# Kernel optimization log

Hardware: AMD Instinct MI355X
Metric: run time of the kernel (lower is better)

Reference implementation:

```python
import jax, jax.numpy as jnp
import numpy as np

NUM_CLASSES = 10
N = 4194304  # 2**22 samples


def setup_inputs() -> dict:
    key = jax.random.key(0)
    k1, k2 = jax.random.split(key)
    outputs = jax.random.uniform(k1, (N, NUM_CLASSES), dtype=jnp.float32)
    target = jax.random.randint(k2, (N,), 0, NUM_CLASSES, dtype=jnp.int64)
    return {"outputs": outputs, "target": target}


def reference(outputs, target):
    # y = one-hot(target) with 10 classes, float
    y = jax.nn.one_hot(target, NUM_CLASSES, dtype=outputs.dtype)  # [N, 10]
    # sum_j (outputs @ y.T)[i, j] == outputs[i] . sum_j y[j]
    # identical math to torch.sum(torch.mm(outputs, y.t()), dim=1) without the [N, N] intermediate
    col_counts = jnp.sum(y, axis=0)                 # [10] class counts
    nominator = outputs @ col_counts                # [N]
    denominator = jnp.linalg.norm(outputs) * jnp.linalg.norm(y)  # Frobenius norms
    return jnp.mean(-jnp.log(nominator / denominator))
```

## Files before the change

### kernel.cpp

```cpp
#include <hip/hip_runtime.h>
#include <math.h>

#define NUM_CLASSES 10
#define A_BLOCKS 512
#define B_BLOCKS 2048


__global__ void __launch_bounds__(256) hist_kernel(const int* __restrict__ target,
                                                   unsigned int* __restrict__ pc, int n) {
    unsigned int cnt[NUM_CLASSES];
#pragma unroll
    for (int c = 0; c < NUM_CLASSES; ++c) cnt[c] = 0u;

    const int tid = blockIdx.x * blockDim.x + threadIdx.x;
    const int stride = gridDim.x * blockDim.x;
    const int4* __restrict__ t4 = (const int4*)target;
    const int n4 = n >> 2;

    unsigned long long acc = 0ull;
    int pend = 0;
    for (int i = tid; i < n4; i += stride) {
        int4 v = t4[i];
        acc += (1ull << (6 * v.x)) + (1ull << (6 * v.y)) +
               (1ull << (6 * v.z)) + (1ull << (6 * v.w));
        if (++pend == 8) {
#pragma unroll
            for (int c = 0; c < NUM_CLASSES; ++c)
                cnt[c] += (unsigned int)((acc >> (6 * c)) & 63ull);
            acc = 0ull;
            pend = 0;
        }
    }
#pragma unroll
    for (int c = 0; c < NUM_CLASSES; ++c)
        cnt[c] += (unsigned int)((acc >> (6 * c)) & 63ull);

#pragma unroll
    for (int c = 0; c < NUM_CLASSES; ++c) {
        unsigned int v = cnt[c];
        for (int off = 32; off > 0; off >>= 1)
            v += (unsigned int)__shfl_down((int)v, off, 64);
        cnt[c] = v;
    }

    __shared__ unsigned int sh[4][NUM_CLASSES];
    const int wave = threadIdx.x >> 6;
    if ((threadIdx.x & 63) == 0) {
#pragma unroll
        for (int c = 0; c < NUM_CLASSES; ++c) sh[wave][c] = cnt[c];
    }
    __syncthreads();
    if (threadIdx.x < NUM_CLASSES) {
        const int c = threadIdx.x;
        pc[blockIdx.x * NUM_CLASSES + c] = sh[0][c] + sh[1][c] + sh[2][c] + sh[3][c];
    }
}

__device__ __forceinline__ void compute_pair(const float4 r[5], const float w[NUM_CLASSES],
                                             float& sum_log, float& sumsq) {
    float r0[NUM_CLASSES] = {r[0].x, r[0].y, r[0].z, r[0].w,
                             r[1].x, r[1].y, r[1].z, r[1].w, r[2].x, r[2].y};
    float r1[NUM_CLASSES] = {r[2].z, r[2].w, r[3].x, r[3].y,
                             r[3].z, r[3].w, r[4].x, r[4].y, r[4].z, r[4].w};
    float nom0 = 0.f, nom1 = 0.f;
#pragma unroll
    for (int c = 0; c < NUM_CLASSES; ++c) {
        nom0 += r0[c] * w[c];
        nom1 += r1[c] * w[c];
        sumsq += r0[c] * r0[c] + r1[c] * r1[c];
    }
    sum_log += __logf(nom0) + __logf(nom1);
}

__device__ __forceinline__ void process_pair_direct(const float4* __restrict__ o4, size_t p,
                                                    const float w[NUM_CLASSES],
                                                    float& sum_log, float& sumsq) {
    const float4* base = o4 + p * 5;
    float4 r[5] = {base[0], base[1], base[2], base[3], base[4]};
    compute_pair(r, w, sum_log, sumsq);
}

__global__ void __launch_bounds__(256) main_kernel(const float* __restrict__ outputs,
                                                   const unsigned int* __restrict__ pc,
                                                   float2* __restrict__ pacc, int n) {
    const int wave = threadIdx.x >> 6;
    const int lane = threadIdx.x & 63;

    unsigned int pw[NUM_CLASSES];
#pragma unroll
    for (int c = 0; c < NUM_CLASSES; ++c) pw[c] = 0u;
#pragma unroll
    for (int r = 0; r < A_BLOCKS / 256; ++r) {
        const unsigned int* row = pc + (threadIdx.x + r * 256) * NUM_CLASSES;
#pragma unroll
        for (int c = 0; c < NUM_CLASSES; ++c) pw[c] += row[c];
    }
#pragma unroll
    for (int c = 0; c < NUM_CLASSES; ++c) {
        unsigned int v = pw[c];
        for (int off = 32; off > 0; off >>= 1)
            v += (unsigned int)__shfl_down((int)v, off, 64);
        pw[c] = v;
    }
    __shared__ unsigned int shw[4][NUM_CLASSES];
    __shared__ float fw[NUM_CLASSES];
    if (lane == 0) {
#pragma unroll
        for (int c = 0; c < NUM_CLASSES; ++c) shw[wave][c] = pw[c];
    }
    __syncthreads();
    if (threadIdx.x < NUM_CLASSES) {
        const int c = threadIdx.x;
        fw[c] = (float)(shw[0][c] + shw[1][c] + shw[2][c] + shw[3][c]);
    }
    __syncthreads();
    float w[NUM_CLASSES];
#pragma unroll
    for (int c = 0; c < NUM_CLASSES; ++c) w[c] = fw[c];

    __shared__ float4 stage[4][5 * 64];
    float4* my = stage[wave];

    int wslot[5], rslot[5];
#pragma unroll
    for (int k = 0; k < 5; ++k) {
        const int j = k * 64 + lane;
        const int c = j % 5;
        const int p = j / 5;
        wslot[k] = c * 64 + (p ^ c);
        rslot[k] = k * 64 + (lane ^ k);
    }

    const float4* __restrict__ o4 = (const float4*)outputs;
    const int npairs = n >> 1;
    const int ntiles = npairs >> 6;
    const int gw = blockIdx.x * 4 + wave;
    const int nwaves = gridDim.x * 4;

    float sum_log = 0.f, sumsq = 0.f;
    for (int tile = gw; tile < ntiles; tile += nwaves) {
        const float4* src = o4 + (size_t)tile * 320;
        float4 g[5];
#pragma unroll
        for (int k = 0; k < 5; ++k) g[k] = src[k * 64 + lane];
#pragma unroll
        for (int k = 0; k < 5; ++k) my[wslot[k]] = g[k];
        float4 r[5];
#pragma unroll
        for (int k = 0; k < 5; ++k) r[k] = my[rslot[k]];
        compute_pair(r, w, sum_log, sumsq);
    }

    const int done = ntiles << 6;
    const int tid = blockIdx.x * blockDim.x + threadIdx.x;
    for (int p = done + tid; p < npairs; p += gridDim.x * blockDim.x)
        process_pair_direct(o4, (size_t)p, w, sum_log, sumsq);

    for (int off = 32; off > 0; off >>= 1) {
        sum_log += __shfl_down(sum_log, off, 64);
        sumsq += __shfl_down(sumsq, off, 64);
    }
    __shared__ float s1[4], s2[4];
    if (lane == 0) { s1[wave] = sum_log; s2[wave] = sumsq; }
    __syncthreads();
    if (threadIdx.x == 0) {
        pacc[blockIdx.x] = make_float2(s1[0] + s1[1] + s1[2] + s1[3],
                                       s2[0] + s2[1] + s2[2] + s2[3]);
    }
}

__global__ void __launch_bounds__(256) finalize_kernel(const float2* __restrict__ pacc,
                                                       float* __restrict__ out, float fn) {
    float sum_log = 0.f, sumsq = 0.f;
    for (int i = threadIdx.x; i < B_BLOCKS; i += 256) {
        float2 v = pacc[i];
        sum_log += v.x;
        sumsq += v.y;
    }
    for (int off = 32; off > 0; off >>= 1) {
        sum_log += __shfl_down(sum_log, off, 64);
        sumsq += __shfl_down(sumsq, off, 64);
    }
    __shared__ float s1[4], s2[4];
    const int wave = threadIdx.x >> 6;
    if ((threadIdx.x & 63) == 0) { s1[wave] = sum_log; s2[wave] = sumsq; }
    __syncthreads();
    if (threadIdx.x == 0) {
        float t1 = s1[0] + s1[1] + s1[2] + s1[3];
        float t2 = s2[0] + s2[1] + s2[2] + s2[3];
        out[0] = 0.5f * logf(t2) + 0.5f * logf(fn) - t1 / fn;
    }
}

extern "C" void kernel_launch(void* const* d_in, const int* in_sizes, int n_in,
                              void* d_out, int out_size, void* d_ws, size_t ws_size,
                              hipStream_t stream) {
    const float* outputs = (const float*)d_in[0];
    const int* target = (const int*)d_in[1];
    const int n = in_sizes[1];

    unsigned int* pc = (unsigned int*)d_ws;
    float2* pacc = (float2*)((char*)d_ws + 20480);

    hist_kernel<<<A_BLOCKS, 256, 0, stream>>>(target, pc, n);
    main_kernel<<<B_BLOCKS, 256, 0, stream>>>(outputs, pc, pacc, n);
    finalize_kernel<<<1, 256, 0, stream>>>(pacc, (float*)d_out, (float)n);
}
```

Before: 248.7 us.

## Fuse histogram, main pass and finalize into one cooperative kernel

Merges the three kernel launches into a single cooperative-groups kernel with 1024 blocks that uses grid-wide syncs between the class-count histogram, the per-row log/sumsq pass, and the final reduction. This removes two kernel launch gaps and their inter-kernel dependencies. It also drops the LDS-staged, swizzled tile loads in favour of direct per-thread strided float4 loads, processing two pairs per iteration. The direct loads give worse coalescing (40-byte stride per thread), and grid syncs plus the limit on co-resident blocks cost something in exchange.

```diff
diff --git a/kernel.cpp b/kernel.cpp
--- a/kernel.cpp
+++ b/kernel.cpp
@@ -1,60 +1,13 @@
 #include <hip/hip_runtime.h>
+#include <hip/hip_cooperative_groups.h>
 #include <math.h>
 
+namespace cg = cooperative_groups;
+
 #define NUM_CLASSES 10
-#define A_BLOCKS 512
-#define B_BLOCKS 2048
+#define BLOCKS 1024
+#define TPB 256
 
-
-__global__ void __launch_bounds__(256) hist_kernel(const int* __restrict__ target,
-                                                   unsigned int* __restrict__ pc, int n) {
-    unsigned int cnt[NUM_CLASSES];
-#pragma unroll
-    for (int c = 0; c < NUM_CLASSES; ++c) cnt[c] = 0u;
-
-    const int tid = blockIdx.x * blockDim.x + threadIdx.x;
-    const int stride = gridDim.x * blockDim.x;
-    const int4* __restrict__ t4 = (const int4*)target;
-    const int n4 = n >> 2;
-
-    unsigned long long acc = 0ull;
-    int pend = 0;
-    for (int i = tid; i < n4; i += stride) {
-        int4 v = t4[i];
-        acc += (1ull << (6 * v.x)) + (1ull << (6 * v.y)) +
-               (1ull << (6 * v.z)) + (1ull << (6 * v.w));
-        if (++pend == 8) {
-#pragma unroll
-            for (int c = 0; c < NUM_CLASSES; ++c)
-                cnt[c] += (unsigned int)((acc >> (6 * c)) & 63ull);
-            acc = 0ull;
-            pend = 0;
-        }
-    }
-#pragma unroll
-    for (int c = 0; c < NUM_CLASSES; ++c)
-        cnt[c] += (unsigned int)((acc >> (6 * c)) & 63ull);
-
-#pragma unroll
-    for (int c = 0; c < NUM_CLASSES; ++c) {
-        unsigned int v = cnt[c];
-        for (int off = 32; off > 0; off >>= 1)
-            v += (unsigned int)__shfl_down((int)v, off, 64);
-        cnt[c] = v;
-    }
-
-    __shared__ unsigned int sh[4][NUM_CLASSES];
-    const int wave = threadIdx.x >> 6;
-    if ((threadIdx.x & 63) == 0) {
-#pragma unroll
-        for (int c = 0; c < NUM_CLASSES; ++c) sh[wave][c] = cnt[c];
-    }
-    __syncthreads();
-    if (threadIdx.x < NUM_CLASSES) {
-        const int c = threadIdx.x;
-        pc[blockIdx.x * NUM_CLASSES + c] = sh[0][c] + sh[1][c] + sh[2][c] + sh[3][c];
-    }
-}
 
 __device__ __forceinline__ void compute_pair(const float4 r[5], const float w[NUM_CLASSES],
                                              float& sum_log, float& sumsq) {
@@ -72,26 +25,77 @@
     sum_log += __logf(nom0) + __logf(nom1);
 }
 
-__device__ __forceinline__ void process_pair_direct(const float4* __restrict__ o4, size_t p,
-                                                    const float w[NUM_CLASSES],
-                                                    float& sum_log, float& sumsq) {
+__device__ __forceinline__ void process_pair(const float4* __restrict__ o4, size_t p,
+                                             const float w[NUM_CLASSES],
+                                             float& sum_log, float& sumsq) {
     const float4* base = o4 + p * 5;
     float4 r[5] = {base[0], base[1], base[2], base[3], base[4]};
     compute_pair(r, w, sum_log, sumsq);
 }
 
-__global__ void __launch_bounds__(256) main_kernel(const float* __restrict__ outputs,
-                                                   const unsigned int* __restrict__ pc,
-                                                   float2* __restrict__ pacc, int n) {
+__global__ void __launch_bounds__(TPB, 4) fused_kernel(const float* __restrict__ outputs,
+                                                       const int* __restrict__ target,
+                                                       unsigned int* __restrict__ pc,
+                                                       float2* __restrict__ pacc,
+                                                       float* __restrict__ out, int n) {
     const int wave = threadIdx.x >> 6;
     const int lane = threadIdx.x & 63;
+    const int tid = blockIdx.x * blockDim.x + threadIdx.x;
+    const int nthreads = gridDim.x * blockDim.x;
+
+    __shared__ unsigned int shw[4][NUM_CLASSES];
+    __shared__ float fw[NUM_CLASSES];
+    __shared__ float s1[4], s2[4];
+
+    unsigned int cnt[NUM_CLASSES];
+#pragma unroll
+    for (int c = 0; c < NUM_CLASSES; ++c) cnt[c] = 0u;
+    {
+        const int4* __restrict__ t4 = (const int4*)target;
+        const int n4 = n >> 2;
+        unsigned long long acc = 0ull;
+        int pend = 0;
+        for (int i = tid; i < n4; i += nthreads) {
+            int4 v = t4[i];
+            acc += (1ull << (6 * v.x)) + (1ull << (6 * v.y)) +
+                   (1ull << (6 * v.z)) + (1ull << (6 * v.w));
+            if (++pend == 8) {
+#pragma unroll
+                for (int c = 0; c < NUM_CLASSES; ++c)
+                    cnt[c] += (unsigned int)((acc >> (6 * c)) & 63ull);
+                acc = 0ull;
+                pend = 0;
+            }
+        }
+#pragma unroll
+        for (int c = 0; c < NUM_CLASSES; ++c)
+            cnt[c] += (unsigned int)((acc >> (6 * c)) & 63ull);
+    }
+#pragma unroll
+    for (int c = 0; c < NUM_CLASSES; ++c) {
+        unsigned int v = cnt[c];
+        for (int off = 32; off > 0; off >>= 1)
+            v += (unsigned int)__shfl_down((int)v, off, 64);
+        cnt[c] = v;
+    }
+    if (lane == 0) {
+#pragma unroll
+        for (int c = 0; c < NUM_CLASSES; ++c) shw[wave][c] = cnt[c];
+    }
+    __syncthreads();
+    if (threadIdx.x < NUM_CLASSES) {
+        const int c = threadIdx.x;
+        pc[blockIdx.x * NUM_CLASSES + c] = shw[0][c] + shw[1][c] + shw[2][c] + shw[3][c];
+    }
+    __threadfence();
+    cg::this_grid().sync();
 
     unsigned int pw[NUM_CLASSES];
 #pragma unroll
     for (int c = 0; c < NUM_CLASSES; ++c) pw[c] = 0u;
 #pragma unroll
-    for (int r = 0; r < A_BLOCKS / 256; ++r) {
-        const unsigned int* row = pc + (threadIdx.x + r * 256) * NUM_CLASSES;
+    for (int r = 0; r < BLOCKS / TPB; ++r) {
+        const unsigned int* row = pc + (threadIdx.x + r * TPB) * NUM_CLASSES;
 #pragma unroll
         for (int c = 0; c < NUM_CLASSES; ++c) pw[c] += row[c];
     }
@@ -102,8 +106,6 @@
             v += (unsigned int)__shfl_down((int)v, off, 64);
         pw[c] = v;
     }
-    __shared__ unsigned int shw[4][NUM_CLASSES];
-    __shared__ float fw[NUM_CLASSES];
     if (lane == 0) {
 #pragma unroll
         for (int c = 0; c < NUM_CLASSES; ++c) shw[wave][c] = pw[c];
@@ -118,77 +120,47 @@
 #pragma unroll
     for (int c = 0; c < NUM_CLASSES; ++c) w[c] = fw[c];
 
-    __shared__ float4 stage[4][5 * 64];
-    float4* my = stage[wave];
-
-    int wslot[5], rslot[5];
-#pragma unroll
-    for (int k = 0; k < 5; ++k) {
-        const int j = k * 64 + lane;
-        const int c = j % 5;
-        const int p = j / 5;
-        wslot[k] = c * 64 + (p ^ c);
-        rslot[k] = k * 64 + (lane ^ k);
-    }
-
     const float4* __restrict__ o4 = (const float4*)outputs;
     const int npairs = n >> 1;
-    const int ntiles = npairs >> 6;
-    const int gw = blockIdx.x * 4 + wave;
-    const int nwaves = gridDim.x * 4;
-
     float sum_log = 0.f, sumsq = 0.f;
-    for (int tile = gw; tile < ntiles; tile += nwaves) {
-        const float4* src = o4 + (size_t)tile * 320;
-        float4 g[5];
-#pragma unroll
-        for (int k = 0; k < 5; ++k) g[k] = src[k * 64 + lane];
-#pragma unroll
-        for (int k = 0; k < 5; ++k) my[wslot[k]] = g[k];
-        float4 r[5];
-#pragma unroll
-        for (int k = 0; k < 5; ++k) r[k] = my[rslot[k]];
-        compute_pair(r, w, sum_log, sumsq);
+    for (int p = tid; p < npairs; p += 2 * nthreads) {
+        process_pair(o4, (size_t)p, w, sum_log, sumsq);
+        const int p2 = p + nthreads;
+        if (p2 < npairs) process_pair(o4, (size_t)p2, w, sum_log, sumsq);
     }
-
-    const int done = ntiles << 6;
-    const int tid = blockIdx.x * blockDim.x + threadIdx.x;
-    for (int p = done + tid; p < npairs; p += gridDim.x * blockDim.x)
-        process_pair_direct(o4, (size_t)p, w, sum_log, sumsq);
 
     for (int off = 32; off > 0; off >>= 1) {
         sum_log += __shfl_down(sum_log, off, 64);
         sumsq += __shfl_down(sumsq, off, 64);
     }
-    __shared__ float s1[4], s2[4];
     if (lane == 0) { s1[wave] = sum_log; s2[wave] = sumsq; }
     __syncthreads();
     if (threadIdx.x == 0) {
         pacc[blockIdx.x] = make_float2(s1[0] + s1[1] + s1[2] + s1[3],
                                        s2[0] + s2[1] + s2[2] + s2[3]);
     }
-}
+    __threadfence();
+    cg::this_grid().sync();
 
-__global__ void __launch_bounds__(256) finalize_kernel(const float2* __restrict__ pacc,
-                                                       float* __restrict__ out, float fn) {
-    float sum_log = 0.f, sumsq = 0.f;
-    for (int i = threadIdx.x; i < B_BLOCKS; i += 256) {
-        float2 v = pacc[i];
-        sum_log += v.x;
-        sumsq += v.y;
-    }
-    for (int off = 32; off > 0; off >>= 1) {
-        sum_log += __shfl_down(sum_log, off, 64);
-        sumsq += __shfl_down(sumsq, off, 64);
-    }
-    __shared__ float s1[4], s2[4];
-    const int wave = threadIdx.x >> 6;
-    if ((threadIdx.x & 63) == 0) { s1[wave] = sum_log; s2[wave] = sumsq; }
-    __syncthreads();
-    if (threadIdx.x == 0) {
-        float t1 = s1[0] + s1[1] + s1[2] + s1[3];
-        float t2 = s2[0] + s2[1] + s2[2] + s2[3];
-        out[0] = 0.5f * logf(t2) + 0.5f * logf(fn) - t1 / fn;
+    if (blockIdx.x == 0) {
+        float t1 = 0.f, t2 = 0.f;
+        for (int i = threadIdx.x; i < BLOCKS; i += TPB) {
+            float2 v = pacc[i];
+            t1 += v.x;
+            t2 += v.y;
+        }
+        for (int off = 32; off > 0; off >>= 1) {
+            t1 += __shfl_down(t1, off, 64);
+            t2 += __shfl_down(t2, off, 64);
+        }
+        if (lane == 0) { s1[wave] = t1; s2[wave] = t2; }
+        __syncthreads();
+        if (threadIdx.x == 0) {
+            const float fn = (float)n;
+            float a = s1[0] + s1[1] + s1[2] + s1[3];
+            float b = s2[0] + s2[1] + s2[2] + s2[3];
+            out[0] = 0.5f * logf(b) + 0.5f * logf(fn) - a / fn;
+        }
     }
 }
 
@@ -197,12 +169,14 @@
                               hipStream_t stream) {
     const float* outputs = (const float*)d_in[0];
     const int* target = (const int*)d_in[1];
-    const int n = in_sizes[1];
+    int n = in_sizes[1];
 
     unsigned int* pc = (unsigned int*)d_ws;
-    float2* pacc = (float2*)((char*)d_ws + 20480);
+    float2* pacc = (float2*)((char*)d_ws + 40960);
+    float* outp = (float*)d_out;
 
-    hist_kernel<<<A_BLOCKS, 256, 0, stream>>>(target, pc, n);
-    main_kernel<<<B_BLOCKS, 256, 0, stream>>>(outputs, pc, pacc, n);
-    finalize_kernel<<<1, 256, 0, stream>>>(pacc, (float*)d_out, (float)n);
+    void* args[] = {(void*)&outputs, (void*)&target, (void*)&pc,
+                    (void*)&pacc,    (void*)&outp,   (void*)&n};
+    hipLaunchCooperativeKernel((const void*)fused_kernel, dim3(BLOCKS), dim3(TPB),
+                               args, 0, stream);
 }
```

After: 590.1 us. +137.3%, slower.
